# Kernel tuning notes

Hardware: AMD Instinct MI355X
Metric: run time of the kernel (lower is better)

## Reference

```python
import jax, jax.numpy as jnp
import numpy as np

N_NODES = 50000
HEADS = 4
CH = 128
NEG_SLOPE = 0.2


def _gatv2_layer(x, src, dst, Wl, Wr, att, bias):
    # x: [N, Fin]; src/dst: [E'] (self-loops already appended)
    N = x.shape[0]
    xl = (x @ Wl).reshape(N, HEADS, CH)   # source-side transform
    xr = (x @ Wr).reshape(N, HEADS, CH)   # target-side transform
    e = jax.nn.leaky_relu(xl[src] + xr[dst], NEG_SLOPE)   # [E', H, C]
    logits = jnp.einsum('ehc,hc->eh', e, att)             # [E', H]
    # segment softmax over incoming edges of each destination node
    m = jax.ops.segment_max(logits, dst, num_segments=N)
    m = jnp.where(jnp.isfinite(m), m, 0.0)
    p = jnp.exp(logits - m[dst])
    denom = jax.ops.segment_sum(p, dst, num_segments=N)
    alpha = p / denom[dst]                                # [E', H]
    out = jax.ops.segment_sum(alpha[:, :, None] * xl[src], dst, num_segments=N)
    return out.reshape(N, HEADS * CH) + bias


def setup_inputs() -> dict:
    key = jax.random.key(0)
    ks = jax.random.split(key, 12)
    E = 400000
    x = jax.random.normal(ks[0], (N_NODES, 55), dtype=jnp.float32)
    edge_index = jax.random.randint(ks[1], (2, E), 0, N_NODES, dtype=jnp.int64)
    s = 0.1
    d1, d2 = 55, HEADS * CH
    return {
        'x': x,
        'edge_index': edge_index,
        'W1l': jax.random.normal(ks[2], (d1, d2), dtype=jnp.float32) * s,
        'W1r': jax.random.normal(ks[3], (d1, d2), dtype=jnp.float32) * s,
        'att1': jax.random.normal(ks[4], (HEADS, CH), dtype=jnp.float32) * s,
        'b1': jnp.zeros((d2,), dtype=jnp.float32),
        'W2l': jax.random.normal(ks[5], (d2, d2), dtype=jnp.float32) * s,
        'W2r': jax.random.normal(ks[6], (d2, d2), dtype=jnp.float32) * s,
        'att2': jax.random.normal(ks[7], (HEADS, CH), dtype=jnp.float32) * s,
        'b2': jnp.zeros((d2,), dtype=jnp.float32),
        'Wc': jax.random.normal(ks[8], (d2, 49), dtype=jnp.float32) * s,
        'bc': jnp.zeros((49,), dtype=jnp.float32),
    }


def reference(x, edge_index, W1l, W1r, att1, b1, W2l, W2r, att2, b2, Wc, bc):
    # add self loops once (PyG GATv2Conv default add_self_loops=True)
    loops = jnp.arange(N_NODES, dtype=edge_index.dtype)
    src = jnp.concatenate([edge_index[0], loops])
    dst = jnp.concatenate([edge_index[1], loops])
    h = _gatv2_layer(x, src, dst, W1l, W1r, att1, b1)
    h = jax.nn.elu(h)  # dropout is identity in eval mode
    h = _gatv2_layer(h, src, dst, W2l, W2r, att2, b2)
    h = jax.nn.elu(h)
    # forward applies conv2 a second time (conv3 unused in source)
    h = _gatv2_layer(h, src, dst, W2l, W2r, att2, b2)
    h = jax.nn.elu(h)
    return h @ Wc + bc
```

## Files before the change

### kernel.cpp

```cpp
#include <hip/hip_runtime.h>
#include <hip/hip_bf16.h>

constexpr int NN   = 50000;
constexpr int EE   = 400000;
constexpr int EP   = 450000;
constexpr int D    = 512;
constexpr int D2   = 1024;
constexpr int F0   = 55;
constexpr int F0P  = 64;
constexpr int OUTC = 49;

typedef __hip_bfloat16 bf16;

using frag_ab = __attribute__((ext_vector_type(8))) short;
using frag_cd = __attribute__((ext_vector_type(4))) float;

__device__ inline void stf(float* p, float v) { *p = v; }
__device__ inline void stf(bf16* p, float v)  { *p = __float2bfloat16(v); }

__device__ inline void unpack8(uint4 u, float* f) {
    unsigned w[4] = {u.x, u.y, u.z, u.w};
    #pragma unroll
    for (int j = 0; j < 4; ++j) {
        __hip_bfloat162 h = *(__hip_bfloat162*)&w[j];
        float2 t = __bfloat1622float2(h);
        f[2 * j] = t.x; f[2 * j + 1] = t.y;
    }
}

template <typename TC>
__global__ __launch_bounds__(256) void gemm_mfma_bt(
    const bf16* __restrict__ A,
    const bf16* __restrict__ Bt,
    TC* __restrict__ C,
    const float* __restrict__ bias,
    int M, int Ncs, int K)
{
    constexpr int BM = 128, BN = 128, BK = 32;
    __shared__ bf16 As[BM * BK];
    __shared__ bf16 Bs[BN * BK];

    int bx = blockIdx.x, by = blockIdx.y;
    if (gridDim.x == 8) {
        int bid = by * 8 + bx;
        bx = (bid >> 3) & 7;
        by = (bid & 7) + ((bid >> 6) << 3);
        if (by * BM >= M) return;
    }

    const int tid  = threadIdx.x;
    const int wave = tid >> 6;
    const int lane = tid & 63;
    const int rowBase = by * BM;
    const int colBase = bx * BN;

    frag_cd acc[4][4] = {};

    int arow0 = rowBase + wave * 32 + (lane >> 2);
    int arow1 = arow0 + 16;
    if (arow0 >= M) arow0 = M - 1;
    if (arow1 >= M) arow1 = M - 1;
    const bf16* gA0 = A + (size_t)arow0 * K + (lane & 3) * 8;
    const bf16* gA1 = A + (size_t)arow1 * K + (lane & 3) * 8;
    const int brow0 = colBase + wave * 32 + (lane >> 2);
    const bf16* gB0 = Bt + (size_t)brow0 * K + (lane & 3) * 8;
    const bf16* gB1 = gB0 + (size_t)16 * K;

    bf16* lA0 = &As[(wave * 32)      * BK];
    bf16* lA1 = &As[(wave * 32 + 16) * BK];
    bf16* lB0 = &Bs[(wave * 32)      * BK];
    bf16* lB1 = &Bs[(wave * 32 + 16) * BK];

    const int m  = lane & 15;
    const int kq = lane >> 4;
    const int wm = (wave >> 1) * 64;
    const int wn = (wave & 1) * 64;

    for (int k0 = 0; k0 < K; k0 += BK) {
        __builtin_amdgcn_global_load_lds(
            (const __attribute__((address_space(1))) void*)(gA0 + k0),
            (__attribute__((address_space(3))) void*)lA0, 16, 0, 0);
        __builtin_amdgcn_global_load_lds(
            (const __attribute__((address_space(1))) void*)(gA1 + k0),
            (__attribute__((address_space(3))) void*)lA1, 16, 0, 0);
        __builtin_amdgcn_global_load_lds(
            (const __attribute__((address_space(1))) void*)(gB0 + k0),
            (__attribute__((address_space(3))) void*)lB0, 16, 0, 0);
        __builtin_amdgcn_global_load_lds(
            (const __attribute__((address_space(1))) void*)(gB1 + k0),
            (__attribute__((address_space(3))) void*)lB1, 16, 0, 0);
        __syncthreads();

        frag_ab a[4], b[4];
        #pragma unroll
        for (int i = 0; i < 4; ++i)
            a[i] = *(const frag_ab*)&As[(wm + i * 16 + m) * BK + kq * 8];
        #pragma unroll
        for (int j = 0; j < 4; ++j)
            b[j] = *(const frag_ab*)&Bs[(wn + j * 16 + m) * BK + kq * 8];
        #pragma unroll
        for (int i = 0; i < 4; ++i)
            #pragma unroll
            for (int j = 0; j < 4; ++j)
                acc[i][j] = __builtin_amdgcn_mfma_f32_16x16x32_bf16(
                    a[i], b[j], acc[i][j], 0, 0, 0);
        __syncthreads();
    }

    #pragma unroll
    for (int i = 0; i < 4; ++i) {
        #pragma unroll
        for (int r = 0; r < 4; ++r) {
            int row = rowBase + wm + i * 16 + kq * 4 + r;
            if (row >= M) continue;
            #pragma unroll
            for (int j = 0; j < 4; ++j) {
                int col = colBase + wn + j * 16 + m;
                if (col >= Ncs) continue;
                float v = acc[i][j][r];
                if (bias) v += bias[col];
                stf(&C[(size_t)row * Ncs + col], v);
            }
        }
    }
}

__global__ void convert_transpose(const float* __restrict__ W, bf16* __restrict__ Wt,
                                  int K, int N) {
    __shared__ float tile[32][33];
    int bn = blockIdx.x * 32, bk = blockIdx.y * 32;
    int tx = threadIdx.x & 31, ty = threadIdx.x >> 5;
    #pragma unroll
    for (int i = 0; i < 32; i += 8)
        tile[ty + i][tx] = W[(size_t)(bk + ty + i) * N + bn + tx];
    __syncthreads();
    #pragma unroll
    for (int i = 0; i < 32; i += 8)
        Wt[(size_t)(bn + ty + i) * K + bk + tx] = __float2bfloat16(tile[tx][ty + i]);
}

__global__ void pad_convert_x(const float* __restrict__ x, bf16* __restrict__ Xp) {
    int idx = blockIdx.x * blockDim.x + threadIdx.x;
    if (idx >= NN * F0P) return;
    int n = idx >> 6, t = idx & 63;
    float v = (t < F0) ? x[n * F0 + t] : 0.f;
    Xp[idx] = __float2bfloat16(v);
}

__global__ void conv_transpose_w1(const float* __restrict__ W, bf16* __restrict__ Wt) {
    int n = blockIdx.x;
    int k = threadIdx.x;
    float v = (k < F0) ? W[(size_t)k * D + n] : 0.f;
    Wt[n * F0P + k] = __float2bfloat16(v);
}

__global__ void conv_transpose_wc(const float* __restrict__ W, bf16* __restrict__ Wt) {
    int n = blockIdx.x;
    for (int k = threadIdx.x; k < D; k += blockDim.x) {
        float v = (n < OUTC) ? W[(size_t)k * OUTC + n] : 0.f;
        Wt[(size_t)n * D + k] = __float2bfloat16(v);
    }
}

__global__ void zero_ints(int* __restrict__ p, int n) {
    int i = blockIdx.x * blockDim.x + threadIdx.x;
    if (i < n) p[i] = 0;
}

__global__ void count_dst(const int* __restrict__ dstIdx, int* __restrict__ cnt) {
    int e = blockIdx.x * blockDim.x + threadIdx.x;
    if (e >= EP) return;
    int dst = (e < EE) ? dstIdx[e] : (e - EE);
    atomicAdd(&cnt[dst], 1);
}

__global__ void scan_blocks(const int* __restrict__ cnt, int* __restrict__ off,
                            int* __restrict__ bsum) {
    __shared__ int sh[1024];
    int i = blockIdx.x * 1024 + threadIdx.x;
    int v = (i < NN) ? cnt[i] : 0;
    sh[threadIdx.x] = v;
    __syncthreads();
    #pragma unroll
    for (int d = 1; d < 1024; d <<= 1) {
        int t = (threadIdx.x >= d) ? sh[threadIdx.x - d] : 0;
        __syncthreads();
        sh[threadIdx.x] += t;
        __syncthreads();
    }
    if (i < NN) off[i] = sh[threadIdx.x] - v;
    if (threadIdx.x == 1023) bsum[blockIdx.x] = sh[1023];
}

__global__ void scan_bsums(int* __restrict__ bsum, int* __restrict__ bbase,
                           int* __restrict__ off, int nb) {
    int lane = threadIdx.x;
    int orig = (lane < nb) ? bsum[lane] : 0;
    int v = orig;
    #pragma unroll
    for (int d = 1; d < 64; d <<= 1) {
        int t = __shfl_up(v, d);
        if (lane >= d) v += t;
    }
    if (lane < nb) bbase[lane] = v - orig;
    if (lane == 63) off[NN] = v;
}

__global__ void add_base(int* __restrict__ off, const int* __restrict__ bbase) {
    int i = blockIdx.x * 1024 + threadIdx.x;
    if (blockIdx.x == 0 || i >= NN) return;
    off[i] += bbase[blockIdx.x];
}

__global__ void fill_srcpos(const int* __restrict__ srcIdx, const int* __restrict__ dstIdx,
                            const int* __restrict__ off, int* __restrict__ cnt,
                            int* __restrict__ srcPos) {
    int e = blockIdx.x * blockDim.x + threadIdx.x;
    if (e >= EP) return;
    int dst = (e < EE) ? dstIdx[e] : (e - EE);
    int src = (e < EE) ? srcIdx[e] : (e - EE);
    int pos = off[dst] + atomicAdd(&cnt[dst], 1);
    srcPos[pos] = src;
}

__global__ __launch_bounds__(256) void gat_edge_fused(
    const bf16* __restrict__ XLR, const float* __restrict__ att,
    const int* __restrict__ off, const int* __restrict__ srcPos,
    const float* __restrict__ bias, bf16* __restrict__ Hout)
{
    int v = blockIdx.x * 4 + (threadIdx.x >> 6);
    if (v >= NN) return;
    int lane = threadIdx.x & 63;

    uint4 ru = *(const uint4*)(XLR + (size_t)v * D2 + D + lane * 8);
    float xr[8]; unpack8(ru, xr);
    const float4* a4 = (const float4*)(att + lane * 8);
    float4 aa = a4[0], ab = a4[1];
    float at[8] = {aa.x, aa.y, aa.z, aa.w, ab.x, ab.y, ab.z, ab.w};

    int s0 = off[v], s1 = off[v + 1];
    float m = -1e30f, den = 0.f;
    float acc[8] = {};

    uint4 lb0 = {0, 0, 0, 0}, lb1 = {0, 0, 0, 0};
    if (s0 < s1)     lb0 = *(const uint4*)(XLR + (size_t)srcPos[s0] * D2 + lane * 8);
    if (s0 + 1 < s1) lb1 = *(const uint4*)(XLR + (size_t)srcPos[s0 + 1] * D2 + lane * 8);

    for (int i = s0; i < s1; ++i) {
        uint4 cur = lb0;
        lb0 = lb1;
        if (i + 2 < s1)
            lb1 = *(const uint4*)(XLR + (size_t)srcPos[i + 2] * D2 + lane * 8);

        float xl[8]; unpack8(cur, xl);
        float s = 0.f;
        #pragma unroll
        for (int j = 0; j < 8; ++j) {
            float t = xl[j] + xr[j];
            t = t > 0.f ? t : 0.2f * t;
            s += t * at[j];
        }
        s += __shfl_xor(s, 1);
        s += __shfl_xor(s, 2);
        s += __shfl_xor(s, 4);
        s += __shfl_xor(s, 8);
        float mn = fmaxf(m, s);
        float scale = __expf(m - mn);
        float p = __expf(s - mn);
        den = den * scale + p;
        #pragma unroll
        for (int j = 0; j < 8; ++j) acc[j] = acc[j] * scale + p * xl[j];
        m = mn;
    }
    float r = 1.f / den;

    const float4* b4 = (const float4*)(bias + lane * 8);
    float4 ba = b4[0], bb = b4[1];
    float bi[8] = {ba.x, ba.y, ba.z, ba.w, bb.x, bb.y, bb.z, bb.w};
    uint4 ou;
    unsigned* ow = (unsigned*)&ou;
    #pragma unroll
    for (int j = 0; j < 4; ++j) {
        float o0 = acc[2 * j] * r + bi[2 * j];
        float o1 = acc[2 * j + 1] * r + bi[2 * j + 1];
        o0 = o0 > 0.f ? o0 : (__expf(o0) - 1.f);
        o1 = o1 > 0.f ? o1 : (__expf(o1) - 1.f);
        __hip_bfloat162 h{__float2bfloat16(o0), __float2bfloat16(o1)};
        ow[j] = *(unsigned*)&h;
    }
    *(uint4*)(Hout + (size_t)v * D + lane * 8) = ou;
}

extern "C" void kernel_launch(void* const* d_in, const int* in_sizes, int n_in,
                              void* d_out, int out_size, void* d_ws, size_t ws_size,
                              hipStream_t stream) {
    const float* x    = (const float*)d_in[0];
    const int*   ei   = (const int*)d_in[1];
    const float* W1l  = (const float*)d_in[2];
    const float* W1r  = (const float*)d_in[3];
    const float* att1 = (const float*)d_in[4];
    const float* b1   = (const float*)d_in[5];
    const float* W2l  = (const float*)d_in[6];
    const float* W2r  = (const float*)d_in[7];
    const float* att2 = (const float*)d_in[8];
    const float* b2   = (const float*)d_in[9];
    const float* Wc   = (const float*)d_in[10];
    const float* bc   = (const float*)d_in[11];
    float* out = (float*)d_out;

    const int* srcIdx = ei;
    const int* dstIdx = ei + EE;

    constexpr int NB = (NN + 1023) / 1024;

    bf16* XLR  = (bf16*)d_ws;
    bf16* Hb   = XLR + (size_t)NN * D2;
    bf16* Xpad = Hb + (size_t)NN * D;
    bf16* W2T  = Xpad + (size_t)NN * F0P;
    bf16* W1T  = W2T + (size_t)D2 * D;
    bf16* WcT  = W1T + (size_t)D2 * F0P;
    int* cnt   = (int*)(WcT + (size_t)128 * D);
    int* cnt2  = cnt + NN;
    int* off   = cnt2 + NN;
    int* srcPos= off + (NN + 1);
    int* bsum  = srcPos + EP;
    int* bbase = bsum + NB;

    zero_ints<<<(2 * NN + 255) / 256, 256, 0, stream>>>(cnt, 2 * NN);
    count_dst<<<(EP + 255) / 256, 256, 0, stream>>>(dstIdx, cnt);
    scan_blocks<<<NB, 1024, 0, stream>>>(cnt, off, bsum);
    scan_bsums<<<1, 64, 0, stream>>>(bsum, bbase, off, NB);
    add_base<<<NB, 1024, 0, stream>>>(off, bbase);
    fill_srcpos<<<(EP + 255) / 256, 256, 0, stream>>>(srcIdx, dstIdx, off, cnt2, srcPos);

    dim3 ctGrid(D / 32, D / 32);
    convert_transpose<<<ctGrid, 256, 0, stream>>>(W2l, W2T, D, D);
    convert_transpose<<<ctGrid, 256, 0, stream>>>(W2r, W2T + (size_t)D * D, D, D);
    conv_transpose_w1<<<D, F0P, 0, stream>>>(W1l, W1T);
    conv_transpose_w1<<<D, F0P, 0, stream>>>(W1r, W1T + (size_t)D * F0P);
    conv_transpose_wc<<<128, 256, 0, stream>>>(Wc, WcT);
    pad_convert_x<<<(NN * F0P + 255) / 256, 256, 0, stream>>>(x, Xpad);

    dim3 gemmGrid(D2 / 128, ((NN + 127) / 128 + 7) / 8 * 8 + 8);
    int nodeBlocks = (NN + 3) / 4;

    gemm_mfma_bt<bf16><<<gemmGrid, 256, 0, stream>>>(Xpad, W1T, XLR, nullptr, NN, D2, F0P);
    gat_edge_fused<<<nodeBlocks, 256, 0, stream>>>(XLR, att1, off, srcPos, b1, Hb);

    for (int rep = 0; rep < 2; ++rep) {
        gemm_mfma_bt<bf16><<<gemmGrid, 256, 0, stream>>>(Hb, W2T, XLR, nullptr, NN, D2, D);
        gat_edge_fused<<<nodeBlocks, 256, 0, stream>>>(XLR, att2, off, srcPos, b2, Hb);
    }

    dim3 gridc(1, (NN + 127) / 128);
    gemm_mfma_bt<float><<<gridc, 256, 0, stream>>>(Hb, WcT, out, bc, NN, OUTC, D);
}
```

Measured before the change: 640.8 us.

## Widen GEMM K-tile with XOR-swizzled LDS and deepen edge gather prefetch

The GEMM K-tile grows from 32 to 64. Global-to-LDS loads now use an XOR swizzle on the 16-byte column group so that fragment reads spread across LDS banks, and the inner loop issues two MFMA sub-steps per tile. This halves the barrier count per K and is meant to cut LDS bank conflicts. Separately, the attention aggregation kernel prefetches four source rows ahead instead of two, giving more memory-level parallelism on the irregular gathers at the cost of extra registers and occupancy pressure.

```diff
diff --git a/kernel.cpp b/kernel.cpp
--- a/kernel.cpp
+++ b/kernel.cpp
@@ -36,7 +36,7 @@
     const float* __restrict__ bias,
     int M, int Ncs, int K)
 {
-    constexpr int BM = 128, BN = 128, BK = 32;
+    constexpr int BM = 128, BN = 128, BK = 64;
     __shared__ bf16 As[BM * BK];
     __shared__ bf16 Bs[BN * BK];
 
@@ -56,54 +56,55 @@
 
     frag_cd acc[4][4] = {};
 
-    int arow0 = rowBase + wave * 32 + (lane >> 2);
-    int arow1 = arow0 + 16;
-    if (arow0 >= M) arow0 = M - 1;
-    if (arow1 >= M) arow1 = M - 1;
-    const bf16* gA0 = A + (size_t)arow0 * K + (lane & 3) * 8;
-    const bf16* gA1 = A + (size_t)arow1 * K + (lane & 3) * 8;
-    const int brow0 = colBase + wave * 32 + (lane >> 2);
-    const bf16* gB0 = Bt + (size_t)brow0 * K + (lane & 3) * 8;
-    const bf16* gB1 = gB0 + (size_t)16 * K;
-
-    bf16* lA0 = &As[(wave * 32)      * BK];
-    bf16* lA1 = &As[(wave * 32 + 16) * BK];
-    bf16* lB0 = &Bs[(wave * 32)      * BK];
-    bf16* lB1 = &Bs[(wave * 32 + 16) * BK];
+    const int lrow = lane >> 3;
+    const int g    = (lane & 7) ^ lrow;
+    int arow[4];
+    #pragma unroll
+    for (int s = 0; s < 4; ++s) {
+        int r = rowBase + wave * 32 + lrow + 8 * s;
+        arow[s] = (r < M) ? r : (M - 1);
+    }
+    const int brow = colBase + wave * 32 + lrow;
 
     const int m  = lane & 15;
     const int kq = lane >> 4;
+    const int sw = m & 7;
     const int wm = (wave >> 1) * 64;
     const int wn = (wave & 1) * 64;
 
     for (int k0 = 0; k0 < K; k0 += BK) {
-        __builtin_amdgcn_global_load_lds(
-            (const __attribute__((address_space(1))) void*)(gA0 + k0),
-            (__attribute__((address_space(3))) void*)lA0, 16, 0, 0);
-        __builtin_amdgcn_global_load_lds(
-            (const __attribute__((address_space(1))) void*)(gA1 + k0),
-            (__attribute__((address_space(3))) void*)lA1, 16, 0, 0);
-        __builtin_amdgcn_global_load_lds(
-            (const __attribute__((address_space(1))) void*)(gB0 + k0),
-            (__attribute__((address_space(3))) void*)lB0, 16, 0, 0);
-        __builtin_amdgcn_global_load_lds(
-            (const __attribute__((address_space(1))) void*)(gB1 + k0),
-            (__attribute__((address_space(3))) void*)lB1, 16, 0, 0);
+        #pragma unroll
+        for (int s = 0; s < 4; ++s) {
+            __builtin_amdgcn_global_load_lds(
+                (const __attribute__((address_space(1))) void*)
+                    (A + (size_t)arow[s] * K + k0 + g * 8),
+                (__attribute__((address_space(3))) void*)
+                    &As[(wave * 32 + 8 * s) * BK], 16, 0, 0);
+            __builtin_amdgcn_global_load_lds(
+                (const __attribute__((address_space(1))) void*)
+                    (Bt + (size_t)(brow + 8 * s) * K + k0 + g * 8),
+                (__attribute__((address_space(3))) void*)
+                    &Bs[(wave * 32 + 8 * s) * BK], 16, 0, 0);
+        }
         __syncthreads();
 
-        frag_ab a[4], b[4];
-        #pragma unroll
-        for (int i = 0; i < 4; ++i)
-            a[i] = *(const frag_ab*)&As[(wm + i * 16 + m) * BK + kq * 8];
-        #pragma unroll
-        for (int j = 0; j < 4; ++j)
-            b[j] = *(const frag_ab*)&Bs[(wn + j * 16 + m) * BK + kq * 8];
-        #pragma unroll
-        for (int i = 0; i < 4; ++i)
+        #pragma unroll
+        for (int kk = 0; kk < 2; ++kk) {
+            const int pg = ((kk * 4 + kq) ^ sw) * 8;
+            frag_ab a[4], b[4];
+            #pragma unroll
+            for (int i = 0; i < 4; ++i)
+                a[i] = *(const frag_ab*)&As[(wm + i * 16 + m) * BK + pg];
             #pragma unroll
             for (int j = 0; j < 4; ++j)
-                acc[i][j] = __builtin_amdgcn_mfma_f32_16x16x32_bf16(
-                    a[i], b[j], acc[i][j], 0, 0, 0);
+                b[j] = *(const frag_ab*)&Bs[(wn + j * 16 + m) * BK + pg];
+            #pragma unroll
+            for (int i = 0; i < 4; ++i)
+                #pragma unroll
+                for (int j = 0; j < 4; ++j)
+                    acc[i][j] = __builtin_amdgcn_mfma_f32_16x16x32_bf16(
+                        a[i], b[j], acc[i][j], 0, 0, 0);
+        }
         __syncthreads();
     }
 
@@ -242,16 +243,10 @@
     float m = -1e30f, den = 0.f;
     float acc[8] = {};
 
-    uint4 lb0 = {0, 0, 0, 0}, lb1 = {0, 0, 0, 0};
-    if (s0 < s1)     lb0 = *(const uint4*)(XLR + (size_t)srcPos[s0] * D2 + lane * 8);
-    if (s0 + 1 < s1) lb1 = *(const uint4*)(XLR + (size_t)srcPos[s0 + 1] * D2 + lane * 8);
-
-    for (int i = s0; i < s1; ++i) {
-        uint4 cur = lb0;
-        lb0 = lb1;
-        if (i + 2 < s1)
-            lb1 = *(const uint4*)(XLR + (size_t)srcPos[i + 2] * D2 + lane * 8);
-
+    auto pre = [&](int idx) -> uint4 {
+        return *(const uint4*)(XLR + (size_t)srcPos[idx] * D2 + lane * 8);
+    };
+    auto step = [&](uint4 cur) {
         float xl[8]; unpack8(cur, xl);
         float s = 0.f;
         #pragma unroll
@@ -271,6 +266,19 @@
         #pragma unroll
         for (int j = 0; j < 8; ++j) acc[j] = acc[j] * scale + p * xl[j];
         m = mn;
+    };
+
+    uint4 p0 = {0,0,0,0}, p1 = p0, p2 = p0, p3 = p0;
+    if (s0 + 0 < s1) p0 = pre(s0 + 0);
+    if (s0 + 1 < s1) p1 = pre(s0 + 1);
+    if (s0 + 2 < s1) p2 = pre(s0 + 2);
+    if (s0 + 3 < s1) p3 = pre(s0 + 3);
+
+    for (int i = s0; i < s1; i += 4) {
+        { step(p0); if (i + 4 < s1) p0 = pre(i + 4); }
+        if (i + 1 < s1) { step(p1); if (i + 5 < s1) p1 = pre(i + 5); }
+        if (i + 2 < s1) { step(p2); if (i + 6 < s1) p2 = pre(i + 6); }
+        if (i + 3 < s1) { step(p3); if (i + 7 < s1) p3 = pre(i + 7); }
     }
     float r = 1.f / den;
 
```

Result: slower. 687.9 us (+7.3%).

## Split each node's edge loop across two waves with shared-memory softmax merge

Applied to the files above, without the earlier changes.

The fused GAT edge kernel now assigns two waves per destination node, each handling alternating incoming edges with its own online-softmax state. The partial max, denominator and accumulators are merged through shared memory after two block barriers. The aim is to double the memory-level parallelism on the latency-bound gather of source rows. The cost is block-wide synchronisation, extra shared-memory traffic and half the waves idling after the merge, and it relies on NN being even since the bounds check was removed.

```diff
diff --git a/kernel.cpp b/kernel.cpp
--- a/kernel.cpp
+++ b/kernel.cpp
@@ -228,9 +228,15 @@
     const int* __restrict__ off, const int* __restrict__ srcPos,
     const float* __restrict__ bias, bf16* __restrict__ Hout)
 {
-    int v = blockIdx.x * 4 + (threadIdx.x >> 6);
-    if (v >= NN) return;
-    int lane = threadIdx.x & 63;
+    __shared__ float mden[2][2][4][2];
+    __shared__ float accb[2][64][8];
+
+    const int wave = threadIdx.x >> 6;
+    const int lane = threadIdx.x & 63;
+    const int nodeSlot = wave >> 1;
+    const int sub = wave & 1;
+    const int v = blockIdx.x * 2 + nodeSlot;
+    const int h = lane >> 4;
 
     uint4 ru = *(const uint4*)(XLR + (size_t)v * D2 + D + lane * 8);
     float xr[8]; unpack8(ru, xr);
@@ -238,19 +244,20 @@
     float4 aa = a4[0], ab = a4[1];
     float at[8] = {aa.x, aa.y, aa.z, aa.w, ab.x, ab.y, ab.z, ab.w};
 
-    int s0 = off[v], s1 = off[v + 1];
+    const int s0 = off[v], s1 = off[v + 1];
     float m = -1e30f, den = 0.f;
     float acc[8] = {};
 
+    int i0 = s0 + sub;
     uint4 lb0 = {0, 0, 0, 0}, lb1 = {0, 0, 0, 0};
-    if (s0 < s1)     lb0 = *(const uint4*)(XLR + (size_t)srcPos[s0] * D2 + lane * 8);
-    if (s0 + 1 < s1) lb1 = *(const uint4*)(XLR + (size_t)srcPos[s0 + 1] * D2 + lane * 8);
-
-    for (int i = s0; i < s1; ++i) {
+    if (i0 < s1)     lb0 = *(const uint4*)(XLR + (size_t)srcPos[i0] * D2 + lane * 8);
+    if (i0 + 2 < s1) lb1 = *(const uint4*)(XLR + (size_t)srcPos[i0 + 2] * D2 + lane * 8);
+
+    for (int i = i0; i < s1; i += 2) {
         uint4 cur = lb0;
         lb0 = lb1;
-        if (i + 2 < s1)
-            lb1 = *(const uint4*)(XLR + (size_t)srcPos[i + 2] * D2 + lane * 8);
+        if (i + 4 < s1)
+            lb1 = *(const uint4*)(XLR + (size_t)srcPos[i + 4] * D2 + lane * 8);
 
         float xl[8]; unpack8(cur, xl);
         float s = 0.f;
@@ -272,7 +279,31 @@
         for (int j = 0; j < 8; ++j) acc[j] = acc[j] * scale + p * xl[j];
         m = mn;
     }
-    float r = 1.f / den;
+
+    if ((lane & 15) == 0) {
+        mden[nodeSlot][sub][h][0] = m;
+        mden[nodeSlot][sub][h][1] = den;
+    }
+    __syncthreads();
+    float mo  = mden[nodeSlot][sub ^ 1][h][0];
+    float dno = mden[nodeSlot][sub ^ 1][h][1];
+    float mstar = fmaxf(m, mo);
+    float fself = __expf(m - mstar);
+    float foth  = __expf(mo - mstar);
+    float denStar = den * fself + dno * foth;
+    #pragma unroll
+    for (int j = 0; j < 8; ++j) acc[j] *= fself;
+
+    if (sub == 1) {
+        #pragma unroll
+        for (int j = 0; j < 8; ++j) accb[nodeSlot][lane][j] = acc[j];
+    }
+    __syncthreads();
+    if (sub == 1) return;
+
+    #pragma unroll
+    for (int j = 0; j < 8; ++j) acc[j] += accb[nodeSlot][lane][j];
+    float r = 1.f / denStar;
 
     const float4* b4 = (const float4*)(bias + lane * 8);
     float4 ba = b4[0], bb = b4[1];
@@ -285,8 +316,8 @@
         float o1 = acc[2 * j + 1] * r + bi[2 * j + 1];
         o0 = o0 > 0.f ? o0 : (__expf(o0) - 1.f);
         o1 = o1 > 0.f ? o1 : (__expf(o1) - 1.f);
-        __hip_bfloat162 h{__float2bfloat16(o0), __float2bfloat16(o1)};
-        ow[j] = *(unsigned*)&h;
+        __hip_bfloat162 hh{__float2bfloat16(o0), __float2bfloat16(o1)};
+        ow[j] = *(unsigned*)&hh;
     }
     *(uint4*)(Hout + (size_t)v * D + lane * 8) = ou;
 }
@@ -342,7 +373,7 @@
     pad_convert_x<<<(NN * F0P + 255) / 256, 256, 0, stream>>>(x, Xpad);
 
     dim3 gemmGrid(D2 / 128, ((NN + 127) / 128 + 7) / 8 * 8 + 8);
-    int nodeBlocks = (NN + 3) / 4;
+    int nodeBlocks = NN / 2;
 
     gemm_mfma_bt<bf16><<<gemmGrid, 256, 0, stream>>>(Xpad, W1T, XLR, nullptr, NN, D2, F0P);
     gat_edge_fused<<<nodeBlocks, 256, 0, stream>>>(XLR, att1, off, srcPos, b1, Hb);
```

New measurement: 686.0 us. 1.07x slower.
